# Performance work log

Hardware: AMD Instinct MI355X
Metric: run time of the kernel (lower is better)

Reference implementation:

```python
import jax, jax.numpy as jnp
import numpy as np

B, S, D_IN, D_OUT, H = 4, 2048, 1024, 1024, 16
HD = D_OUT // H  # 64


def setup_inputs() -> dict:
    key = jax.random.key(0)
    ks = jax.random.split(key, 6)
    s = 1.0 / np.sqrt(D_IN)
    return {
        "x": jax.random.normal(ks[0], (B, S, D_IN), dtype=jnp.float32),
        "Wq": jax.random.uniform(ks[1], (D_IN, D_OUT), jnp.float32, -s, s),
        "Wk": jax.random.uniform(ks[2], (D_IN, D_OUT), jnp.float32, -s, s),
        "Wv": jax.random.uniform(ks[3], (D_IN, D_OUT), jnp.float32, -s, s),
        "Wo": jax.random.uniform(ks[4], (D_OUT, D_OUT), jnp.float32, -s, s),
        "bo": jax.random.uniform(ks[5], (D_OUT,), jnp.float32, -s, s),
    }


def reference(x, Wq, Wk, Wv, Wo, bo):
    b, s, _ = x.shape
    # QKV projections -> [b, H, s, hd]
    def split_heads(t):
        return t.reshape(b, s, H, HD).transpose(0, 2, 1, 3)
    q = split_heads(x @ Wq)
    k = split_heads(x @ Wk)
    v = split_heads(x @ Wv)
    # attention scores [b, H, s, s]
    scores = jnp.einsum("bhqd,bhkd->bhqk", q, k)
    causal = jnp.triu(jnp.ones((s, s), dtype=bool), k=1)
    scores = jnp.where(causal, -jnp.inf, scores)
    attn = jax.nn.softmax(scores / np.sqrt(HD), axis=-1)
    ctx = jnp.einsum("bhqk,bhkd->bhqd", attn, v)
    ctx = ctx.transpose(0, 2, 1, 3).reshape(b, s, D_OUT)
    return ctx @ Wo + bo
```

## Files before the change

kernel.cpp:

```cpp
#include <hip/hip_runtime.h>

typedef __attribute__((ext_vector_type(8))) short bf16x8;
typedef __attribute__((ext_vector_type(4))) float f32x4;
typedef __attribute__((ext_vector_type(2))) float f32x2;
typedef __attribute__((ext_vector_type(4))) unsigned uint4v;

#define SM_C 0.18033688011112042f
#define MFMA16 __builtin_amdgcn_mfma_f32_16x16x32_bf16

__device__ __forceinline__ unsigned short f2bf(float f) {
  unsigned u = __builtin_bit_cast(unsigned, f);
  u += 0x7fffu + ((u >> 16) & 1u);
  return (unsigned short)(u >> 16);
}

__device__ __forceinline__ unsigned cvtpk(float lo, float hi) {
  unsigned r;
  asm volatile("v_cvt_pk_bf16_f32 %0, %1, %2" : "=v"(r) : "v"(lo), "v"(hi));
  return r;
}

__device__ __forceinline__ f32x2 pk_fma(f32x2 a, f32x2 b, f32x2 c) {
  f32x2 d;
  asm("v_pk_fma_f32 %0, %1, %2, %3" : "=v"(d) : "v"(a), "v"(b), "v"(c));
  return d;
}
__device__ __forceinline__ f32x2 pk_add(f32x2 a, f32x2 b) {
  f32x2 d;
  asm("v_pk_add_f32 %0, %1, %2" : "=v"(d) : "v"(a), "v"(b));
  return d;
}
__device__ __forceinline__ f32x2 pk_mul(f32x2 a, f32x2 b) {
  f32x2 d;
  asm("v_pk_mul_f32 %0, %1, %2" : "=v"(d) : "v"(a), "v"(b));
  return d;
}

__device__ __forceinline__ void gload16(const void* g, void* lds) {
  __builtin_amdgcn_global_load_lds(
      (const __attribute__((address_space(1))) void*)g,
      (__attribute__((address_space(3))) void*)lds, 16, 0, 0);
}

#define BARRIER __builtin_amdgcn_s_barrier()
#define LGKM0 asm volatile("s_waitcnt lgkmcnt(0)" ::: "memory")

__global__ __launch_bounds__(256) void cvt_x(const float* __restrict__ in,
                                             unsigned short* __restrict__ out,
                                             int n4) {
  int i = blockIdx.x * 256 + threadIdx.x;
  int stride = gridDim.x * 256;
  for (; i < n4; i += stride) {
    float4 v = ((const float4*)in)[i];
    unsigned short o0 = f2bf(v.x), o1 = f2bf(v.y), o2 = f2bf(v.z), o3 = f2bf(v.w);
    unsigned long long packed = (unsigned long long)o0 | ((unsigned long long)o1 << 16) |
                                ((unsigned long long)o2 << 32) | ((unsigned long long)o3 << 48);
    ((unsigned long long*)out)[i] = packed;
  }
}

__global__ __launch_bounds__(256) void transpose_w4(const float* __restrict__ W0,
                                                    const float* __restrict__ W1,
                                                    const float* __restrict__ W2,
                                                    const float* __restrict__ W3,
                                                    unsigned short* __restrict__ WT) {
  __shared__ float tile[32][33];
  const int z = blockIdx.z;
  const float* W = (z == 0) ? W0 : (z == 1) ? W1 : (z == 2) ? W2 : W3;
  unsigned short* WTo = WT + (size_t)z * 1048576;
  int bx = blockIdx.x, by = blockIdx.y;
  int x = bx * 32 + threadIdx.x;
  for (int i = 0; i < 4; ++i) {
    int r = threadIdx.y + i * 8;
    tile[r][threadIdx.x] = W[(by * 32 + r) * 1024 + x];
  }
  __syncthreads();
  int nx = by * 32 + threadIdx.x;
  for (int i = 0; i < 4; ++i) {
    int r = threadIdx.y + i * 8;
    WTo[(long)(bx * 32 + r) * 1024 + nx] = f2bf(tile[threadIdx.x][r]);
  }
}

template <int NR, int MODE>
__global__ __launch_bounds__(512, 1) void gemm3b(const unsigned short* __restrict__ A,
                                                 const unsigned short* __restrict__ BT,
                                                 unsigned short* __restrict__ Cb,
                                                 float* __restrict__ Cf,
                                                 const float* __restrict__ bias,
                                                 int M, int N, int K) {
  constexpr int BN = NR * 64;
  __shared__ alignas(16) unsigned short As[3][256 * 64];
  __shared__ alignas(16) unsigned short Bs[2][BN * 64];

  const int nbn = N / BN;
  const int tmg = (M / 256) / 8;
  const int cc = blockIdx.x >> 3, xc = blockIdx.x & 7;
  const int tm = xc * tmg + cc / nbn, tn = cc % nbn;

  const int t = threadIdx.x, l = t & 63, wid = t >> 6;
  const int wm = wid >> 2, wn = wid & 3;
  const int lr = l & 15, lg = l >> 4;

  f32x4 acc[8][NR] = {};

  const int sq = t >> 3;
  const int sslot8 = ((t & 7) ^ (sq & 7)) * 8;
  const unsigned short* Ath = A + ((long)tm * 256 + sq) * K + sslot8;
  const unsigned short* Bth = BT + ((long)tn * BN + sq) * K + sslot8;
  const int ldsoff = sq * 64 + (t & 7) * 8;

#define STGA(buf, q, kt) \
  gload16(Ath + (long)((q)*64) * K + (kt)*64, &As[buf][(q)*4096 + ldsoff])
#define STGB(buf, u, kt) \
  gload16(Bth + (long)((u)*64) * K + (kt)*64, &Bs[buf][(u)*4096 + ldsoff])

  const int NT = K >> 6;
#pragma unroll
  for (int q = 0; q < 4; ++q) STGA(0, q, 0);
#pragma unroll
  for (int u = 0; u < NR; ++u) STGB(0, u, 0);
#pragma unroll
  for (int q = 0; q < 4; ++q) STGA(1, q, 1);

  const int offk0 = (lg ^ (lr & 7)) * 8;
  const int offk1 = ((4 + lg) ^ (lr & 7)) * 8;
  const int arow0 = (wm * 128 + lr) * 64;
  const int brow0 = (wn * (NR * 16) + lr) * 64;

#define DS_A(MH)                                                   \
  _Pragma("unroll") for (int m_ = 0; m_ < 4; ++m_) {               \
    const unsigned short* ap_ = Ac + arow0 + ((MH)*4 + m_) * 1024; \
    af[m_][0] = *(const bf16x8*)(ap_ + offk0);                     \
    af[m_][1] = *(const bf16x8*)(ap_ + offk1);                     \
  }
#define DS_B_ALL                                          \
  _Pragma("unroll") for (int n_ = 0; n_ < NR; ++n_) {     \
    const unsigned short* bp_ = Bc + brow0 + n_ * 1024;   \
    bfr[n_][0] = *(const bf16x8*)(bp_ + offk0);           \
    bfr[n_][1] = *(const bf16x8*)(bp_ + offk1);           \
  }
#define MM(MH)                                                              \
  __builtin_amdgcn_s_setprio(1);                                            \
  _Pragma("unroll") for (int m_ = 0; m_ < 4; ++m_)                          \
  _Pragma("unroll") for (int n_ = 0; n_ < NR; ++n_) {                       \
    acc[(MH)*4 + m_][n_] = MFMA16(af[m_][0], bfr[n_][0],                    \
                                  acc[(MH)*4 + m_][n_], 0, 0, 0);           \
    acc[(MH)*4 + m_][n_] = MFMA16(af[m_][1], bfr[n_][1],                    \
                                  acc[(MH)*4 + m_][n_], 0, 0, 0);           \
  }                                                                         \
  __builtin_amdgcn_s_setprio(0);

  int cur3 = 0;
  int stg3 = 2;
  for (int tt = 0; tt < NT; ++tt) {
    const unsigned short* Ac = As[cur3];
    const unsigned short* Bc = Bs[tt & 1];

    bf16x8 af[4][2];
    bf16x8 bfr[NR][2];

    if (tt == NT - 1) asm volatile("s_waitcnt vmcnt(0)" ::: "memory");
    else              asm volatile("s_waitcnt vmcnt(4)" ::: "memory");
    BARRIER;
    DS_A(0);
    DS_B_ALL;
    if (tt + 1 < NT) {
      const int nbB = (tt + 1) & 1;
#pragma unroll
      for (int u = 0; u < NR; ++u) STGB(nbB, u, tt + 1);
    }
    BARRIER;
    LGKM0;
    MM(0);

    DS_A(1);
    if (tt + 2 < NT) {
#pragma unroll
      for (int q = 0; q < 4; ++q) STGA(stg3, q, tt + 2);
    }
    BARRIER;
    LGKM0;
    MM(1);

    cur3 = (cur3 == 2) ? 0 : cur3 + 1;
    stg3 = (stg3 == 2) ? 0 : stg3 + 1;
  }
#undef DS_A
#undef DS_B_ALL
#undef MM
#undef STGA
#undef STGB

  const long crow = (long)tm * 256 + wm * 128;
  const int ccol = tn * BN + wn * (NR * 16);

  if constexpr (MODE == 1) {
#pragma unroll
    for (int m = 0; m < 8; ++m)
#pragma unroll
      for (int n = 0; n < NR; ++n)
#pragma unroll
        for (int r = 0; r < 4; ++r) {
          long row = crow + m * 16 + lg * 4 + r;
          int col = ccol + n * 16 + lr;
          Cf[row * N + col] = acc[m][n][r] + bias[col];
        }
  } else {
    if (tn < 16) {
      unsigned short* plane = Cb + ((tn < 8) ? 0 : 8388608);
      const int pc = ccol - ((tn < 8) ? 0 : 1024);
#pragma unroll
      for (int m = 0; m < 8; ++m)
#pragma unroll
        for (int n = 0; n < NR; ++n)
#pragma unroll
          for (int r = 0; r < 4; ++r) {
            long row = crow + m * 16 + lg * 4 + r;
            plane[row * 1024 + pc + n * 16 + lr] = f2bf(acc[m][n][r]);
          }
    } else {
      unsigned short* VtW = Cb + 16777216;
      const int bq = (tm >> 3) << 4;
      const int sbase = (tm & 7) * 256 + wm * 128;
#pragma unroll
      for (int m = 0; m < 8; ++m) {
        const int lwb = (m * 16 + lg * 4) & 63;
        const int stt = (sbase + m * 16 + lg * 4) >> 6;
        const int vp0 = (lwb & 32) | (((lwb >> 2) & 3) << 3) | (((lwb >> 4) & 1) << 2);
#pragma unroll
        for (int n = 0; n < NR; ++n) {
          const int vcol = ccol + n * 16 + lr - 2048;
          const long vtrow = (long)(bq + (vcol >> 6)) * 64 + (vcol & 63);
          unsigned long long pk4 =
              (unsigned long long)f2bf(acc[m][n][0]) |
              ((unsigned long long)f2bf(acc[m][n][1]) << 16) |
              ((unsigned long long)f2bf(acc[m][n][2]) << 32) |
              ((unsigned long long)f2bf(acc[m][n][3]) << 48);
          *(unsigned long long*)(VtW + vtrow * 2048 + stt * 64 + vp0) = pk4;
        }
      }
    }
  }
}

template <int TWO>
__device__ __forceinline__ void attn_tile(
    const unsigned short* __restrict__ Kc, const unsigned short* __restrict__ Vc,
    int lr, int lg, bool mask0, bool mask1, int kv0, int q0row, int q1row,
    const bf16x8 (&qf)[2][2], f32x4 (&cacc)[2][4], float (&m_r)[2], float (&l_r)[2]) {
  constexpr int S0 = TWO ? 0 : 1;
  f32x4 p[2][4];
#pragma unroll
  for (int s = S0; s < 2; ++s)
#pragma unroll
    for (int g = 0; g < 4; ++g) p[s][g] = f32x4{0.f, 0.f, 0.f, 0.f};

  __builtin_amdgcn_s_setprio(1);
#pragma unroll
  for (int g = 0; g < 4; ++g) {
    const int key = g * 16 + lr;
    const int swz = (key & 7) << 3;
#pragma unroll
    for (int c = 0; c < 2; ++c) {
      bf16x8 kf = *(const bf16x8*)(Kc + key * 64 + ((c * 32 + lg * 8) ^ swz));
#pragma unroll
      for (int s = S0; s < 2; ++s)
        p[s][g] = MFMA16(kf, qf[s][c], p[s][g], 0, 0, 0);
    }
  }
  __builtin_amdgcn_s_setprio(0);

  if (TWO && mask0) {
#pragma unroll
    for (int g = 0; g < 4; ++g)
#pragma unroll
      for (int r = 0; r < 4; ++r)
        if (kv0 + g * 16 + lg * 4 + r > q0row) p[0][g][r] = -1e30f;
  }
  if (mask1) {
#pragma unroll
    for (int g = 0; g < 4; ++g)
#pragma unroll
      for (int r = 0; r < 4; ++r)
        if (kv0 + g * 16 + lg * 4 + r > q1row) p[1][g][r] = -1e30f;
  }

  const f32x2 C2 = {SM_C, SM_C};
  unsigned pk[2][4][2];
#pragma unroll
  for (int s = S0; s < 2; ++s) {
    float mloc = p[s][0][0];
#pragma unroll
    for (int g = 0; g < 4; ++g)
#pragma unroll
      for (int r = 0; r < 4; ++r) mloc = fmaxf(mloc, p[s][g][r]);
    mloc = fmaxf(mloc, __shfl_xor(mloc, 16));
    mloc = fmaxf(mloc, __shfl_xor(mloc, 32));
    const bool defer = __all(mloc <= m_r[s] + 44.0f);
    const float mn = defer ? m_r[s] : fmaxf(m_r[s], mloc);
    f32x2 nmc2;
    nmc2[0] = nmc2[1] = -mn * SM_C;
    f32x2 ex[4][2];
#pragma unroll
    for (int g = 0; g < 4; ++g) {
      f32x2 lo = {p[s][g][0], p[s][g][1]};
      f32x2 hi = {p[s][g][2], p[s][g][3]};
      ex[g][0] = pk_fma(lo, C2, nmc2);
      ex[g][1] = pk_fma(hi, C2, nmc2);
      ex[g][0][0] = __builtin_amdgcn_exp2f(ex[g][0][0]);
      ex[g][0][1] = __builtin_amdgcn_exp2f(ex[g][0][1]);
      ex[g][1][0] = __builtin_amdgcn_exp2f(ex[g][1][0]);
      ex[g][1][1] = __builtin_amdgcn_exp2f(ex[g][1][1]);
    }
    f32x2 r0 = pk_add(ex[0][0], ex[0][1]);
    f32x2 r1 = pk_add(ex[1][0], ex[1][1]);
    f32x2 r2 = pk_add(ex[2][0], ex[2][1]);
    f32x2 r3 = pk_add(ex[3][0], ex[3][1]);
    f32x2 r01 = pk_add(r0, r1);
    f32x2 r23 = pk_add(r2, r3);
    f32x2 rv = pk_add(r01, r23);
    float rs = rv[0] + rv[1];
    rs += __shfl_xor(rs, 16);
    rs += __shfl_xor(rs, 32);
    if (defer) {
      l_r[s] += rs;
    } else {
      float alpha = __builtin_amdgcn_exp2f((m_r[s] - mn) * SM_C);
      l_r[s] = l_r[s] * alpha + rs;
      m_r[s] = mn;
      float alq[4];
#pragma unroll
      for (int r = 0; r < 4; ++r) alq[r] = __shfl(alpha, lg * 20 + r);
      f32x2 alo = {alq[0], alq[1]};
      f32x2 ahi = {alq[2], alq[3]};
#pragma unroll
      for (int n = 0; n < 4; ++n) {
        f32x2 clo = {cacc[s][n][0], cacc[s][n][1]};
        f32x2 chi = {cacc[s][n][2], cacc[s][n][3]};
        clo = pk_mul(clo, alo);
        chi = pk_mul(chi, ahi);
        cacc[s][n][0] = clo[0]; cacc[s][n][1] = clo[1];
        cacc[s][n][2] = chi[0]; cacc[s][n][3] = chi[1];
      }
    }
#pragma unroll
    for (int g = 0; g < 4; ++g) {
      pk[s][g][0] = cvtpk(ex[g][0][0], ex[g][0][1]);
      pk[s][g][1] = cvtpk(ex[g][1][0], ex[g][1][1]);
    }
  }

#pragma unroll
  for (int sl = 0; sl < 2; ++sl) {
    bf16x8 vf[4];
#pragma unroll
    for (int n = 0; n < 4; ++n) {
      const int hd = n * 16 + lr;
      vf[n] = *(const bf16x8*)(Vc + hd * 64 + ((sl * 32 + lg * 8) ^ ((hd & 7) << 3)));
    }
    __builtin_amdgcn_s_setprio(1);
#pragma unroll
    for (int s = S0; s < 2; ++s) {
      uint4v pw = {pk[s][2 * sl][0], pk[s][2 * sl][1], pk[s][2 * sl + 1][0], pk[s][2 * sl + 1][1]};
      bf16x8 pa = __builtin_bit_cast(bf16x8, pw);
#pragma unroll
      for (int n = 0; n < 4; ++n)
        cacc[s][n] = MFMA16(pa, vf[n], cacc[s][n], 0, 0, 0);
    }
    __builtin_amdgcn_s_setprio(0);
  }
}

__global__ __launch_bounds__(256, 4) void flash_attn(const unsigned short* __restrict__ Qp,
                                                     const unsigned short* __restrict__ Kp,
                                                     const unsigned short* __restrict__ Vt,
                                                     unsigned short* __restrict__ Ctx) {
  __shared__ alignas(16) unsigned short Ks[2][64 * 64];
  __shared__ alignas(16) unsigned short Vs[2][64 * 64];
  const int bid = blockIdx.x;
  const int qt = bid >> 6;
  const int bh = bid & 63;
  const int b = bh >> 4, h = bh & 15;
  const int t = threadIdx.x, l = t & 63, w = t >> 6;
  const int lr = l & 15, lg = l >> 4;
  const long rowbase = (long)b * 2048;
  const int colbase = h * 64;
  const int q0 = qt * 64 + w * 16;
  const int q1 = (31 - qt) * 64 + w * 16;
  const int q0row = q0 + lr, q1row = q1 + lr;
  const int nkv = 32 - qt;

  bf16x8 qf[2][2];
#pragma unroll
  for (int c = 0; c < 2; ++c) {
    qf[0][c] = *(const bf16x8*)(Qp + (rowbase + q0 + lr) * 1024 + colbase + c * 32 + lg * 8);
    qf[1][c] = *(const bf16x8*)(Qp + (rowbase + q1 + lr) * 1024 + colbase + c * 32 + lg * 8);
  }

  f32x4 cacc[2][4];
  float m_r[2], l_r[2];
#pragma unroll
  for (int s = 0; s < 2; ++s) {
    m_r[s] = -1e30f;
    l_r[s] = 0.f;
#pragma unroll
    for (int n = 0; n < 4; ++n) cacc[s][n] = f32x4{0.f, 0.f, 0.f, 0.f};
  }

  const int srow = w * 16 + (l >> 3);
  const int scol = (l & 7) * 8;
  const int kswz = scol ^ ((srow & 7) << 3);
  const unsigned short* kp = Kp + (rowbase + srow) * 1024 + colbase + kswz;
  const unsigned short* vp = Vt + ((long)(bh * 64 + srow)) * 2048 + kswz;
  unsigned short* ksd0 = &Ks[0][(w * 16) * 64];
  unsigned short* vsd0 = &Vs[0][(w * 16) * 64];

#define STAGE(buf)                                    \
  do {                                                \
    gload16(kp, ksd0 + (buf) * 4096);                 \
    gload16(kp + 8 * 1024, ksd0 + (buf) * 4096 + 512);\
    gload16(vp, vsd0 + (buf) * 4096);                 \
    gload16(vp + 8 * 2048, vsd0 + (buf) * 4096 + 512);\
    kp += 64 * 1024;                                  \
    vp += 64;                                         \
  } while (0)

#define TILE_WAIT(j)                                                          \
  do {                                                                        \
    if ((j) == nkv - 1) asm volatile("s_waitcnt vmcnt(0)" ::: "memory");      \
    else                asm volatile("s_waitcnt vmcnt(4)" ::: "memory");      \
    asm volatile("s_barrier" ::: "memory");                                   \
  } while (0)

  STAGE(0);
  STAGE(1);

  int j = 0;
  for (; j <= qt; ++j) {
    const int cur = j & 1;
    TILE_WAIT(j);
    attn_tile<1>(Ks[cur], Vs[cur], lr, lg, j == qt, false, j * 64, q0row, q1row,
                 qf, cacc, m_r, l_r);
    asm volatile("s_barrier" ::: "memory");
    if (j + 2 < nkv) STAGE(cur);
  }
  for (; j < nkv; ++j) {
    const int cur = j & 1;
    TILE_WAIT(j);
    attn_tile<0>(Ks[cur], Vs[cur], lr, lg, false, j == nkv - 1, j * 64, q0row, q1row,
                 qf, cacc, m_r, l_r);
    asm volatile("s_barrier" ::: "memory");
    if (j + 2 < nkv) STAGE(cur);
  }
#undef STAGE
#undef TILE_WAIT

#pragma unroll
  for (int s = 0; s < 2; ++s) {
    float invl = 1.f / l_r[s];
    float ilq[4];
#pragma unroll
    for (int r = 0; r < 4; ++r) ilq[r] = __shfl(invl, lg * 20 + r);
    const int qs = (s == 0) ? q0 : q1;
#pragma unroll
    for (int n = 0; n < 4; ++n)
#pragma unroll
      for (int r = 0; r < 4; ++r) {
        long row = rowbase + qs + lg * 4 + r;
        Ctx[row * 1024 + colbase + n * 16 + lr] = f2bf(cacc[s][n][r] * ilq[r]);
      }
  }
}

extern "C" void kernel_launch(void* const* d_in, const int* in_sizes, int n_in,
                              void* d_out, int out_size, void* d_ws, size_t ws_size,
                              hipStream_t stream) {
  (void)in_sizes; (void)n_in; (void)out_size; (void)ws_size;
  const float* x  = (const float*)d_in[0];
  const float* Wq = (const float*)d_in[1];
  const float* Wk = (const float*)d_in[2];
  const float* Wv = (const float*)d_in[3];
  const float* Wo = (const float*)d_in[4];
  const float* bo = (const float*)d_in[5];
  float* out = (float*)d_out;

  unsigned short* ws = (unsigned short*)d_ws;
  unsigned short* xb  = ws;
  unsigned short* WqT = ws + 8388608;
  unsigned short* WoT = WqT + 3145728;
  unsigned short* QKV = WqT + 4194304;
  unsigned short* Qp  = QKV;
  unsigned short* Kp  = QKV + 8388608;
  unsigned short* Vt  = QKV + 16777216;
  unsigned short* Ctx = QKV + 25165824;

  cvt_x<<<2048, 256, 0, stream>>>(x, xb, 8192 * 1024 / 4);

  dim3 tb(32, 8), tg(32, 32, 4);
  transpose_w4<<<tg, tb, 0, stream>>>(Wq, Wk, Wv, Wo, WqT);

  gemm3b<2, 0><<<768, 512, 0, stream>>>(xb, WqT, QKV, nullptr, nullptr,
                                        8192, 3072, 1024);

  flash_attn<<<1024, 256, 0, stream>>>(Qp, Kp, Vt, Ctx);

  gemm3b<2, 1><<<256, 512, 0, stream>>>(Ctx, WoT, nullptr, out, bo,
                                        8192, 1024, 1024);
}
```

Measured before the change: 156.9 us.

## Widen QKV GEMM tile to NR=3 with per-column-block plane routing

The QKV projection GEMM now uses a wider N tile (NR=3, 512 blocks instead of 768), so a single tile can straddle the Q/K/V plane boundaries. The epilogue therefore picks the destination plane per 16-column group instead of per tile. Wider tiles are meant to raise reuse of the A operand and cut the number of blocks, at the cost of more accumulator registers. Separately, the softmax row-max reduction becomes a tree instead of a serial chain to shorten the dependency chain.

Result: faster. 151.3 us (-3.6%).

```diff
diff --git a/kernel.cpp b/kernel.cpp
--- a/kernel.cpp
+++ b/kernel.cpp
@@ -207,31 +207,32 @@
           Cf[row * N + col] = acc[m][n][r] + bias[col];
         }
   } else {
-    if (tn < 16) {
-      unsigned short* plane = Cb + ((tn < 8) ? 0 : 8388608);
-      const int pc = ccol - ((tn < 8) ? 0 : 1024);
-#pragma unroll
-      for (int m = 0; m < 8; ++m)
-#pragma unroll
-        for (int n = 0; n < NR; ++n)
+#pragma unroll
+    for (int n = 0; n < NR; ++n) {
+      const int colg = ccol + n * 16;
+      const int plane = colg >> 10;
+      if (plane < 2) {
+        unsigned short* pl = Cb + (size_t)plane * 8388608;
+        const int pc = (colg & 1023) + lr;
+#pragma unroll
+        for (int m = 0; m < 8; ++m)
 #pragma unroll
           for (int r = 0; r < 4; ++r) {
             long row = crow + m * 16 + lg * 4 + r;
-            plane[row * 1024 + pc + n * 16 + lr] = f2bf(acc[m][n][r]);
+            pl[row * 1024 + pc] = f2bf(acc[m][n][r]);
           }
-    } else {
-      unsigned short* VtW = Cb + 16777216;
-      const int bq = (tm >> 3) << 4;
-      const int sbase = (tm & 7) * 256 + wm * 128;
-#pragma unroll
-      for (int m = 0; m < 8; ++m) {
-        const int lwb = (m * 16 + lg * 4) & 63;
-        const int stt = (sbase + m * 16 + lg * 4) >> 6;
-        const int vp0 = (lwb & 32) | (((lwb >> 2) & 3) << 3) | (((lwb >> 4) & 1) << 2);
-#pragma unroll
-        for (int n = 0; n < NR; ++n) {
-          const int vcol = ccol + n * 16 + lr - 2048;
-          const long vtrow = (long)(bq + (vcol >> 6)) * 64 + (vcol & 63);
+      } else {
+        unsigned short* VtW = Cb + 16777216;
+        const int bq = (tm >> 3) << 4;
+        const int sbase = ((tm & 7) << 8) + wm * 128;
+        const int vcol = (colg & 1023) + lr;
+        const long vtrow = (long)(bq + (vcol >> 6)) * 64 + (vcol & 63);
+#pragma unroll
+        for (int m = 0; m < 8; ++m) {
+          const int srow_ = sbase + m * 16 + lg * 4;
+          const int lwb = srow_ & 63;
+          const int stt = srow_ >> 6;
+          const int vp0 = (lwb & 32) | (((lwb >> 2) & 3) << 3) | (((lwb >> 4) & 1) << 2);
           unsigned long long pk4 =
               (unsigned long long)f2bf(acc[m][n][0]) |
               ((unsigned long long)f2bf(acc[m][n][1]) << 16) |
@@ -290,11 +291,15 @@
   unsigned pk[2][4][2];
 #pragma unroll
   for (int s = S0; s < 2; ++s) {
-    float mloc = p[s][0][0];
-#pragma unroll
-    for (int g = 0; g < 4; ++g)
-#pragma unroll
-      for (int r = 0; r < 4; ++r) mloc = fmaxf(mloc, p[s][g][r]);
+    f32x4 t0, t1;
+#pragma unroll
+    for (int r = 0; r < 4; ++r) {
+      t0[r] = fmaxf(p[s][0][r], p[s][1][r]);
+      t1[r] = fmaxf(p[s][2][r], p[s][3][r]);
+    }
+#pragma unroll
+    for (int r = 0; r < 4; ++r) t0[r] = fmaxf(t0[r], t1[r]);
+    float mloc = fmaxf(fmaxf(t0[0], t0[1]), fmaxf(t0[2], t0[3]));
     mloc = fmaxf(mloc, __shfl_xor(mloc, 16));
     mloc = fmaxf(mloc, __shfl_xor(mloc, 32));
     const bool defer = __all(mloc <= m_r[s] + 44.0f);
@@ -500,7 +505,7 @@
   dim3 tb(32, 8), tg(32, 32, 4);
   transpose_w4<<<tg, tb, 0, stream>>>(Wq, Wk, Wv, Wo, WqT);
 
-  gemm3b<2, 0><<<768, 512, 0, stream>>>(xb, WqT, QKV, nullptr, nullptr,
+  gemm3b<3, 0><<<512, 512, 0, stream>>>(xb, WqT, QKV, nullptr, nullptr,
                                         8192, 3072, 1024);
 
   flash_attn<<<1024, 256, 0, stream>>>(Qp, Kp, Vt, Ctx);
```
